# Kernel optimization log

Measured on AMD Instinct MI355X. Metric: run time of the kernel, lower is better.

The kernel has to match this reference:

```python
import jax, jax.numpy as jnp
from jax import lax
import numpy as np

B, T, D, H, L = 512, 1024, 5, 128, 16


def _u(key, shape, fan):
    bound = 1.0 / np.sqrt(fan)
    return jax.random.uniform(key, shape, jnp.float32, -bound, bound)


def setup_inputs() -> dict:
    key = jax.random.key(0)
    ks = jax.random.split(key, 16)
    return {
        "x": jax.random.normal(ks[0], (B, T, D), jnp.float32),
        # encoder GRU (PyTorch layout: rows ordered [reset; update; new])
        "enc_W_ih": _u(ks[1], (3 * H, D), H),
        "enc_W_hh": _u(ks[2], (3 * H, H), H),
        "enc_b_ih": _u(ks[3], (3 * H,), H),
        "enc_b_hh": _u(ks[4], (3 * H,), H),
        # encoder_fc: hidden -> latent
        "enc_fc_W": _u(ks[5], (L, H), H),
        "enc_fc_b": _u(ks[6], (L,), H),
        # decoder_fc: latent -> hidden
        "dec_fc_W": _u(ks[7], (H, L), L),
        "dec_fc_b": _u(ks[8], (H,), L),
        # decoder GRU (input size = hidden_dim)
        "dec_W_ih": _u(ks[9], (3 * H, H), H),
        "dec_W_hh": _u(ks[10], (3 * H, H), H),
        "dec_b_ih": _u(ks[11], (3 * H,), H),
        "dec_b_hh": _u(ks[12], (3 * H,), H),
        # output_fc: hidden -> input_dim
        "out_W": _u(ks[13], (D, H), H),
        "out_b": _u(ks[14], (D,), H),
    }


def _gru_step(W_hh, b_hh, h, xp):
    # xp: precomputed input projection [B, 3H]; PyTorch GRU cell math
    hp = h @ W_hh.T + b_hh
    r = jax.nn.sigmoid(xp[:, :H] + hp[:, :H])
    zg = jax.nn.sigmoid(xp[:, H:2 * H] + hp[:, H:2 * H])
    n = jnp.tanh(xp[:, 2 * H:] + r * hp[:, 2 * H:])
    return (1.0 - zg) * n + zg * h


def reference(x, enc_W_ih, enc_W_hh, enc_b_ih, enc_b_hh, enc_fc_W, enc_fc_b,
              dec_fc_W, dec_fc_b, dec_W_ih, dec_W_hh, dec_b_ih, dec_b_hh,
              out_W, out_b):
    b, t, _ = x.shape
    # ---- encode: precompute all input projections, scan the recurrence ----
    xp_enc = jnp.einsum('btd,gd->tbg', x, enc_W_ih) + enc_b_ih  # [T,B,3H]
    h0 = jnp.zeros((b, H), x.dtype)
    h_n, _ = lax.scan(lambda h, xp: (_gru_step(enc_W_hh, enc_b_hh, h, xp), None),
                      h0, xp_enc)
    z = h_n @ enc_fc_W.T + enc_fc_b  # [B,L]
    # ---- decode: constant repeated input => one shared input projection ----
    h_dec_in = z @ dec_fc_W.T + dec_fc_b  # [B,H]
    xp_dec = h_dec_in @ dec_W_ih.T + dec_b_ih  # [B,3H], same every step

    def dec_step(h, _):
        h_new = _gru_step(dec_W_hh, dec_b_hh, h, xp_dec)
        return h_new, h_new

    _, hs = lax.scan(dec_step, jnp.zeros((b, H), x.dtype), None, length=t)  # [T,B,H]
    recon = jnp.einsum('tbh,dh->btd', hs, out_W) + out_b  # [B,T,D]
    return recon, z
```

## Files before the change

### kernel.cpp

```cpp
#include <hip/hip_runtime.h>

#define Hd 128
#define HF 64
#define Tn 1024
#define Dn 5
#define Ln 16
#define Bn 512

__device__ __forceinline__ float sigm(float x) { return 1.0f / (1.0f + __expf(-x)); }
__device__ __forceinline__ float tanh_fast(float x) { return 1.0f - 2.0f / (1.0f + __expf(2.0f * x)); }

__global__ __launch_bounds__(512, 2) void gru_ae_kernel(
    const float* __restrict__ x,
    const float* __restrict__ eWih, const float* __restrict__ eWhh,
    const float* __restrict__ ebih, const float* __restrict__ ebhh,
    const float* __restrict__ efcW, const float* __restrict__ efcb,
    const float* __restrict__ dfcW, const float* __restrict__ dfcb,
    const float* __restrict__ dWih, const float* __restrict__ dWhh,
    const float* __restrict__ dbih, const float* __restrict__ dbhh,
    const float* __restrict__ oW, const float* __restrict__ ob,
    float* __restrict__ out)
{
    __shared__ __align__(16) float henc[2][2][Hd];
    __shared__ __align__(16) float hs[2][32][Hd];
    __shared__ __align__(16) float hdi[2][Hd];
    __shared__ float zl[2][Ln];

    const int tid  = threadIdx.x;
    const int bl   = tid >> 8;
    const int loc  = tid & 255;
    const int j    = loc >> 1;
    const int kk   = loc & 1;
    const int b    = blockIdx.x * 2 + bl;
    const int koff = kk * HF;

    float4 wr[16], wz[16], wn[16];
    {
        const float4* p0 = (const float4*)(eWhh + (size_t)j * Hd + koff);
        const float4* p1 = (const float4*)(eWhh + (size_t)(Hd + j) * Hd + koff);
        const float4* p2 = (const float4*)(eWhh + (size_t)(2 * Hd + j) * Hd + koff);
#pragma unroll
        for (int k = 0; k < 16; ++k) { wr[k] = p0[k]; wz[k] = p1[k]; wn[k] = p2[k]; }
    }
    float wir[5], wiz[5], win[5];
#pragma unroll
    for (int d = 0; d < 5; ++d) {
        wir[d] = eWih[(size_t)j * Dn + d];
        wiz[d] = eWih[(size_t)(Hd + j) * Dn + d];
        win[d] = eWih[(size_t)(2 * Hd + j) * Dn + d];
    }
    float bR = ebih[j] + ebhh[j];
    float bZ = ebih[Hd + j] + ebhh[Hd + j];
    float bihn = ebih[2 * Hd + j];
    float bhhn = ebhh[2 * Hd + j];

    if (loc < Hd) { henc[0][bl][loc] = 0.f; henc[1][bl][loc] = 0.f; }
    __syncthreads();

    float h_self = 0.f;
    int p = 0;
    const float* xrow = x + (size_t)b * Tn * Dn;
    float xc0 = xrow[0], xc1 = xrow[1], xc2 = xrow[2], xc3 = xrow[3], xc4 = xrow[4];

#pragma unroll 1
    for (int t = 0; t < Tn; ++t) {
        const int tn = (t + 1 < Tn) ? (t + 1) : t;
        const float* xq = xrow + tn * Dn;
        float nx0 = xq[0], nx1 = xq[1], nx2 = xq[2], nx3 = xq[3], nx4 = xq[4];

        float xpr = wir[0]*xc0 + wir[1]*xc1 + wir[2]*xc2 + wir[3]*xc3 + wir[4]*xc4;
        float xpz = wiz[0]*xc0 + wiz[1]*xc1 + wiz[2]*xc2 + wiz[3]*xc3 + wiz[4]*xc4;
        float xpn = win[0]*xc0 + win[1]*xc1 + win[2]*xc2 + win[3]*xc3 + win[4]*xc4;

        const float4* hv = (const float4*)&henc[p][bl][koff];
        float ar = 0.f, az = 0.f, an = 0.f;
#pragma unroll
        for (int k = 0; k < 16; ++k) {
            float4 h4 = hv[k];
            ar = fmaf(wr[k].x, h4.x, ar); az = fmaf(wz[k].x, h4.x, az); an = fmaf(wn[k].x, h4.x, an);
            ar = fmaf(wr[k].y, h4.y, ar); az = fmaf(wz[k].y, h4.y, az); an = fmaf(wn[k].y, h4.y, an);
            ar = fmaf(wr[k].z, h4.z, ar); az = fmaf(wz[k].z, h4.z, az); an = fmaf(wn[k].z, h4.z, an);
            ar = fmaf(wr[k].w, h4.w, ar); az = fmaf(wz[k].w, h4.w, az); an = fmaf(wn[k].w, h4.w, an);
        }
        ar += __shfl_xor(ar, 1); az += __shfl_xor(az, 1); an += __shfl_xor(an, 1);
        float r  = sigm(xpr + ar + bR);
        float zg = sigm(xpz + az + bZ);
        float n  = tanh_fast(xpn + bihn + r * (an + bhhn));
        float hnew = fmaf(zg, h_self - n, n);
        h_self = hnew;
        if (!kk) henc[p ^ 1][bl][j] = hnew;
        xc0 = nx0; xc1 = nx1; xc2 = nx2; xc3 = nx3; xc4 = nx4;
        __syncthreads();
        p ^= 1;
    }

    if (loc < Ln) {
        const float4* wp = (const float4*)(efcW + (size_t)loc * Hd);
        const float4* hv = (const float4*)henc[p][bl];
        float acc = efcb[loc];
#pragma unroll
        for (int k = 0; k < 32; ++k) {
            float4 w4 = wp[k], h4 = hv[k];
            acc = fmaf(w4.x, h4.x, fmaf(w4.y, h4.y, fmaf(w4.z, h4.z, fmaf(w4.w, h4.w, acc))));
        }
        out[(size_t)Bn * Tn * Dn + (size_t)b * Ln + loc] = acc;
        zl[bl][loc] = acc;
    }
    __syncthreads();

    if (loc < Hd) {
        const float4* wp = (const float4*)(dfcW + (size_t)loc * Ln);
        float acc = dfcb[loc];
#pragma unroll
        for (int l = 0; l < 4; ++l) {
            float4 w4 = wp[l];
            acc = fmaf(w4.x, zl[bl][4*l+0], acc);
            acc = fmaf(w4.y, zl[bl][4*l+1], acc);
            acc = fmaf(w4.z, zl[bl][4*l+2], acc);
            acc = fmaf(w4.w, zl[bl][4*l+3], acc);
        }
        hdi[bl][loc] = acc;
    }
    __syncthreads();

    float xdr, xdz, xdn;
    {
        const float4* p0 = (const float4*)(dWih + (size_t)j * Hd + koff);
        const float4* p1 = (const float4*)(dWih + (size_t)(Hd + j) * Hd + koff);
        const float4* p2 = (const float4*)(dWih + (size_t)(2 * Hd + j) * Hd + koff);
#pragma unroll
        for (int k = 0; k < 16; ++k) { wr[k] = p0[k]; wz[k] = p1[k]; wn[k] = p2[k]; }
        const float4* hv = (const float4*)&hdi[bl][koff];
        float a0 = 0.f, a1 = 0.f, a2 = 0.f;
#pragma unroll
        for (int k = 0; k < 16; ++k) {
            float4 h4 = hv[k];
            a0 = fmaf(wr[k].x, h4.x, a0); a1 = fmaf(wz[k].x, h4.x, a1); a2 = fmaf(wn[k].x, h4.x, a2);
            a0 = fmaf(wr[k].y, h4.y, a0); a1 = fmaf(wz[k].y, h4.y, a1); a2 = fmaf(wn[k].y, h4.y, a2);
            a0 = fmaf(wr[k].z, h4.z, a0); a1 = fmaf(wz[k].z, h4.z, a1); a2 = fmaf(wn[k].z, h4.z, a2);
            a0 = fmaf(wr[k].w, h4.w, a0); a1 = fmaf(wz[k].w, h4.w, a1); a2 = fmaf(wn[k].w, h4.w, a2);
        }
        a0 += __shfl_xor(a0, 1); a1 += __shfl_xor(a1, 1); a2 += __shfl_xor(a2, 1);
        xdr = a0 + dbih[j];
        xdz = a1 + dbih[Hd + j];
        xdn = a2 + dbih[2 * Hd + j];
    }

    {
        const float4* p0 = (const float4*)(dWhh + (size_t)j * Hd + koff);
        const float4* p1 = (const float4*)(dWhh + (size_t)(Hd + j) * Hd + koff);
        const float4* p2 = (const float4*)(dWhh + (size_t)(2 * Hd + j) * Hd + koff);
#pragma unroll
        for (int k = 0; k < 16; ++k) { wr[k] = p0[k]; wz[k] = p1[k]; wn[k] = p2[k]; }
    }
    bR = dbhh[j];
    bZ = dbhh[Hd + j];
    bhhn = dbhh[2 * Hd + j];

    if (loc < Hd) hs[bl][31][loc] = 0.f;
    h_self = 0.f;
    __syncthreads();

#pragma unroll 1
    for (int s0 = 0; s0 < Tn; s0 += 32) {
#pragma unroll 1
        for (int ss = 0; ss < 32; ++ss) {
            const int ip = (ss + 31) & 31;
            const float4* hv = (const float4*)&hs[bl][ip][koff];
            float ar = 0.f, az = 0.f, an = 0.f;
#pragma unroll
            for (int k = 0; k < 16; ++k) {
                float4 h4 = hv[k];
                ar = fmaf(wr[k].x, h4.x, ar); az = fmaf(wz[k].x, h4.x, az); an = fmaf(wn[k].x, h4.x, an);
                ar = fmaf(wr[k].y, h4.y, ar); az = fmaf(wz[k].y, h4.y, az); an = fmaf(wn[k].y, h4.y, an);
                ar = fmaf(wr[k].z, h4.z, ar); az = fmaf(wz[k].z, h4.z, az); an = fmaf(wn[k].z, h4.z, an);
                ar = fmaf(wr[k].w, h4.w, ar); az = fmaf(wz[k].w, h4.w, az); an = fmaf(wn[k].w, h4.w, an);
            }
            ar += __shfl_xor(ar, 1); az += __shfl_xor(az, 1); an += __shfl_xor(an, 1);
            float r  = sigm(xdr + ar + bR);
            float zg = sigm(xdz + az + bZ);
            float n  = tanh_fast(xdn + r * (an + bhhn));
            float hnew = fmaf(zg, h_self - n, n);
            h_self = hnew;
            if (!kk) hs[bl][ss][j] = hnew;
            __syncthreads();
        }

        if (tid < 320) {
            const int rowp = tid / 160, o = tid % 160;
            const int i = o / 5, d = o % 5;
            const float4* wrow = (const float4*)(oW + (size_t)d * Hd);
            const float4* hrow = (const float4*)hs[rowp][i];
            float ac0 = ob[d], ac1 = 0.f;
#pragma unroll
            for (int q = 0; q < 32; q += 2) {
                const int qa = (q + i) & 31, qb = (q + 1 + i) & 31;
                float4 ha = hrow[qa], wa = wrow[qa];
                float4 hb = hrow[qb], wb = wrow[qb];
                ac0 = fmaf(wa.x, ha.x, fmaf(wa.y, ha.y, fmaf(wa.z, ha.z, fmaf(wa.w, ha.w, ac0))));
                ac1 = fmaf(wb.x, hb.x, fmaf(wb.y, hb.y, fmaf(wb.z, hb.z, fmaf(wb.w, hb.w, ac1))));
            }
            out[((size_t)(blockIdx.x * 2 + rowp) * Tn + s0 + i) * Dn + d] = ac0 + ac1;
        }
        __syncthreads();
    }
}

extern "C" void kernel_launch(void* const* d_in, const int* in_sizes, int n_in,
                              void* d_out, int out_size, void* d_ws, size_t ws_size,
                              hipStream_t stream) {
    const float* x    = (const float*)d_in[0];
    const float* eWih = (const float*)d_in[1];
    const float* eWhh = (const float*)d_in[2];
    const float* ebih = (const float*)d_in[3];
    const float* ebhh = (const float*)d_in[4];
    const float* efcW = (const float*)d_in[5];
    const float* efcb = (const float*)d_in[6];
    const float* dfcW = (const float*)d_in[7];
    const float* dfcb = (const float*)d_in[8];
    const float* dWih = (const float*)d_in[9];
    const float* dWhh = (const float*)d_in[10];
    const float* dbih = (const float*)d_in[11];
    const float* dbhh = (const float*)d_in[12];
    const float* oW   = (const float*)d_in[13];
    const float* ob   = (const float*)d_in[14];
    float* out = (float*)d_out;

    gru_ae_kernel<<<dim3(Bn / 2), dim3(512), 0, stream>>>(
        x, eWih, eWhh, ebih, ebhh, efcW, efcb, dfcW, dfcb,
        dWih, dWhh, dbih, dbhh, oW, ob, out);
}
```

Baseline: 2.448 ms.

## Split GRU hidden dot products four ways with one batch row per block

Each block now handles a single batch row instead of two. The 128-wide recurrent dot product is split across 4 lanes instead of 2, which halves the per-thread weight registers and doubles the grid to 512 blocks. LDS rows are padded with a GF/CF skew to avoid bank conflicts on the quarter-sliced reads, and the 5-dim input projection is spread across the lanes and reduced together with the recurrent sums. The aim is a shorter per-step serial FMA chain and more waves per EU. In exchange, each step needs an extra shuffle-reduction stage, and block-level barriers are paid for half as many rows per block.

```diff
diff --git a/kernel.cpp b/kernel.cpp
--- a/kernel.cpp
+++ b/kernel.cpp
@@ -1,16 +1,23 @@
 #include <hip/hip_runtime.h>
 
 #define Hd 128
-#define HF 64
 #define Tn 1024
 #define Dn 5
 #define Ln 16
 #define Bn 512
+#define QP 36
+#define HP4 144
+#define GF(f) ((f) + (((f) >> 5) << 2))
+#define CF(q) (QP * ((q) >> 3) + 4 * ((q) & 7))
 
 __device__ __forceinline__ float sigm(float x) { return 1.0f / (1.0f + __expf(-x)); }
 __device__ __forceinline__ float tanh_fast(float x) { return 1.0f - 2.0f / (1.0f + __expf(2.0f * x)); }
 
-__global__ __launch_bounds__(512, 2) void gru_ae_kernel(
+#define RED4(v) { v += __shfl_xor(v, 1); v += __shfl_xor(v, 2); }
+
+__global__ __launch_bounds__(512)
+__attribute__((amdgpu_waves_per_eu(4, 4)))
+void gru_ae_kernel(
     const float* __restrict__ x,
     const float* __restrict__ eWih, const float* __restrict__ eWhh,
     const float* __restrict__ ebih, const float* __restrict__ ebhh,
@@ -21,105 +28,105 @@
     const float* __restrict__ oW, const float* __restrict__ ob,
     float* __restrict__ out)
 {
-    __shared__ __align__(16) float henc[2][2][Hd];
-    __shared__ __align__(16) float hs[2][32][Hd];
-    __shared__ __align__(16) float hdi[2][Hd];
-    __shared__ float zl[2][Ln];
-
-    const int tid  = threadIdx.x;
-    const int bl   = tid >> 8;
-    const int loc  = tid & 255;
-    const int j    = loc >> 1;
-    const int kk   = loc & 1;
-    const int b    = blockIdx.x * 2 + bl;
-    const int koff = kk * HF;
-
-    float4 wr[16], wz[16], wn[16];
+    __shared__ __align__(16) float henc[2][HP4];
+    __shared__ __align__(16) float hs[32][HP4];
+    __shared__ __align__(16) float hdi[HP4];
+    __shared__ float zl[Ln];
+
+    const int tid = threadIdx.x;
+    const int j   = tid >> 2;
+    const int kq  = tid & 3;
+    const int b   = blockIdx.x;
+    const int koff = kq * 32;
+    const int klds = kq * QP;
+
+    float4 wr[8], wz[8], wn[8];
     {
         const float4* p0 = (const float4*)(eWhh + (size_t)j * Hd + koff);
         const float4* p1 = (const float4*)(eWhh + (size_t)(Hd + j) * Hd + koff);
         const float4* p2 = (const float4*)(eWhh + (size_t)(2 * Hd + j) * Hd + koff);
 #pragma unroll
-        for (int k = 0; k < 16; ++k) { wr[k] = p0[k]; wz[k] = p1[k]; wn[k] = p2[k]; }
-    }
-    float wir[5], wiz[5], win[5];
-#pragma unroll
-    for (int d = 0; d < 5; ++d) {
-        wir[d] = eWih[(size_t)j * Dn + d];
-        wiz[d] = eWih[(size_t)(Hd + j) * Dn + d];
-        win[d] = eWih[(size_t)(2 * Hd + j) * Dn + d];
-    }
+        for (int k = 0; k < 8; ++k) { wr[k] = p0[k]; wz[k] = p1[k]; wn[k] = p2[k]; }
+    }
+    const int d0s = (kq == 1) ? 2 : (kq == 2) ? 4 : 0;
+    const int inc = (kq < 2) ? 1 : 0;
+    const float m0 = (kq < 3) ? 1.f : 0.f, m1 = (kq < 2) ? 1.f : 0.f;
+    float wxr0 = m0 * eWih[(size_t)j * Dn + d0s];
+    float wxr1 = m1 * eWih[(size_t)j * Dn + d0s + inc];
+    float wxz0 = m0 * eWih[(size_t)(Hd + j) * Dn + d0s];
+    float wxz1 = m1 * eWih[(size_t)(Hd + j) * Dn + d0s + inc];
+    float wxn0 = m0 * eWih[(size_t)(2 * Hd + j) * Dn + d0s];
+    float wxn1 = m1 * eWih[(size_t)(2 * Hd + j) * Dn + d0s + inc];
+
     float bR = ebih[j] + ebhh[j];
     float bZ = ebih[Hd + j] + ebhh[Hd + j];
     float bihn = ebih[2 * Hd + j];
     float bhhn = ebhh[2 * Hd + j];
 
-    if (loc < Hd) { henc[0][bl][loc] = 0.f; henc[1][bl][loc] = 0.f; }
+    if (tid < Hd) { henc[0][GF(tid)] = 0.f; henc[1][GF(tid)] = 0.f; }
     __syncthreads();
 
     float h_self = 0.f;
     int p = 0;
     const float* xrow = x + (size_t)b * Tn * Dn;
-    float xc0 = xrow[0], xc1 = xrow[1], xc2 = xrow[2], xc3 = xrow[3], xc4 = xrow[4];
+    float xc0 = xrow[d0s], xc1 = xrow[d0s + inc];
 
 #pragma unroll 1
     for (int t = 0; t < Tn; ++t) {
-        const int tn = (t + 1 < Tn) ? (t + 1) : t;
-        const float* xq = xrow + tn * Dn;
-        float nx0 = xq[0], nx1 = xq[1], nx2 = xq[2], nx3 = xq[3], nx4 = xq[4];
-
-        float xpr = wir[0]*xc0 + wir[1]*xc1 + wir[2]*xc2 + wir[3]*xc3 + wir[4]*xc4;
-        float xpz = wiz[0]*xc0 + wiz[1]*xc1 + wiz[2]*xc2 + wiz[3]*xc3 + wiz[4]*xc4;
-        float xpn = win[0]*xc0 + win[1]*xc1 + win[2]*xc2 + win[3]*xc3 + win[4]*xc4;
-
-        const float4* hv = (const float4*)&henc[p][bl][koff];
-        float ar = 0.f, az = 0.f, an = 0.f;
-#pragma unroll
-        for (int k = 0; k < 16; ++k) {
+        const int off = ((t + 1 < Tn) ? (t + 1) : (Tn - 1)) * Dn;
+        float nx0 = xrow[off + d0s], nx1 = xrow[off + d0s + inc];
+
+        const float4* hv = (const float4*)&henc[p][klds];
+        float ar = 0.f, az = 0.f, nh = 0.f;
+#pragma unroll
+        for (int k = 0; k < 8; ++k) {
             float4 h4 = hv[k];
-            ar = fmaf(wr[k].x, h4.x, ar); az = fmaf(wz[k].x, h4.x, az); an = fmaf(wn[k].x, h4.x, an);
-            ar = fmaf(wr[k].y, h4.y, ar); az = fmaf(wz[k].y, h4.y, az); an = fmaf(wn[k].y, h4.y, an);
-            ar = fmaf(wr[k].z, h4.z, ar); az = fmaf(wz[k].z, h4.z, az); an = fmaf(wn[k].z, h4.z, an);
-            ar = fmaf(wr[k].w, h4.w, ar); az = fmaf(wz[k].w, h4.w, az); an = fmaf(wn[k].w, h4.w, an);
-        }
-        ar += __shfl_xor(ar, 1); az += __shfl_xor(az, 1); an += __shfl_xor(an, 1);
-        float r  = sigm(xpr + ar + bR);
-        float zg = sigm(xpz + az + bZ);
-        float n  = tanh_fast(xpn + bihn + r * (an + bhhn));
+            ar = fmaf(wr[k].x, h4.x, ar); az = fmaf(wz[k].x, h4.x, az); nh = fmaf(wn[k].x, h4.x, nh);
+            ar = fmaf(wr[k].y, h4.y, ar); az = fmaf(wz[k].y, h4.y, az); nh = fmaf(wn[k].y, h4.y, nh);
+            ar = fmaf(wr[k].z, h4.z, ar); az = fmaf(wz[k].z, h4.z, az); nh = fmaf(wn[k].z, h4.z, nh);
+            ar = fmaf(wr[k].w, h4.w, ar); az = fmaf(wz[k].w, h4.w, az); nh = fmaf(wn[k].w, h4.w, nh);
+        }
+        ar = fmaf(wxr0, xc0, fmaf(wxr1, xc1, ar));
+        az = fmaf(wxz0, xc0, fmaf(wxz1, xc1, az));
+        float nx = fmaf(wxn0, xc0, wxn1 * xc1);
+        RED4(ar); RED4(az); RED4(nh); RED4(nx);
+        float r  = sigm(ar + bR);
+        float zg = sigm(az + bZ);
+        float n  = tanh_fast(nx + bihn + r * (nh + bhhn));
         float hnew = fmaf(zg, h_self - n, n);
         h_self = hnew;
-        if (!kk) henc[p ^ 1][bl][j] = hnew;
-        xc0 = nx0; xc1 = nx1; xc2 = nx2; xc3 = nx3; xc4 = nx4;
+        if (!kq) henc[p ^ 1][GF(j)] = hnew;
+        xc0 = nx0; xc1 = nx1;
         __syncthreads();
         p ^= 1;
     }
 
-    if (loc < Ln) {
-        const float4* wp = (const float4*)(efcW + (size_t)loc * Hd);
-        const float4* hv = (const float4*)henc[p][bl];
-        float acc = efcb[loc];
-#pragma unroll
-        for (int k = 0; k < 32; ++k) {
-            float4 w4 = wp[k], h4 = hv[k];
+    if (tid < Ln) {
+        const float4* wp = (const float4*)(efcW + (size_t)tid * Hd);
+        float acc = efcb[tid];
+#pragma unroll
+        for (int q = 0; q < 32; ++q) {
+            float4 w4 = wp[q];
+            float4 h4 = *(const float4*)&henc[p][CF(q)];
             acc = fmaf(w4.x, h4.x, fmaf(w4.y, h4.y, fmaf(w4.z, h4.z, fmaf(w4.w, h4.w, acc))));
         }
-        out[(size_t)Bn * Tn * Dn + (size_t)b * Ln + loc] = acc;
-        zl[bl][loc] = acc;
-    }
-    __syncthreads();
-
-    if (loc < Hd) {
-        const float4* wp = (const float4*)(dfcW + (size_t)loc * Ln);
-        float acc = dfcb[loc];
+        out[(size_t)Bn * Tn * Dn + (size_t)b * Ln + tid] = acc;
+        zl[tid] = acc;
+    }
+    __syncthreads();
+
+    if (tid < Hd) {
+        const float4* wp = (const float4*)(dfcW + (size_t)tid * Ln);
+        float acc = dfcb[tid];
 #pragma unroll
         for (int l = 0; l < 4; ++l) {
             float4 w4 = wp[l];
-            acc = fmaf(w4.x, zl[bl][4*l+0], acc);
-            acc = fmaf(w4.y, zl[bl][4*l+1], acc);
-            acc = fmaf(w4.z, zl[bl][4*l+2], acc);
-            acc = fmaf(w4.w, zl[bl][4*l+3], acc);
-        }
-        hdi[bl][loc] = acc;
+            acc = fmaf(w4.x, zl[4 * l + 0], acc);
+            acc = fmaf(w4.y, zl[4 * l + 1], acc);
+            acc = fmaf(w4.z, zl[4 * l + 2], acc);
+            acc = fmaf(w4.w, zl[4 * l + 3], acc);
+        }
+        hdi[GF(tid)] = acc;
     }
     __syncthreads();
 
@@ -129,21 +136,22 @@
         const float4* p1 = (const float4*)(dWih + (size_t)(Hd + j) * Hd + koff);
         const float4* p2 = (const float4*)(dWih + (size_t)(2 * Hd + j) * Hd + koff);
 #pragma unroll
-        for (int k = 0; k < 16; ++k) { wr[k] = p0[k]; wz[k] = p1[k]; wn[k] = p2[k]; }
-        const float4* hv = (const float4*)&hdi[bl][koff];
+        for (int k = 0; k < 8; ++k) { wr[k] = p0[k]; wz[k] = p1[k]; wn[k] = p2[k]; }
+        const float4* hv = (const float4*)&hdi[klds];
         float a0 = 0.f, a1 = 0.f, a2 = 0.f;
 #pragma unroll
-        for (int k = 0; k < 16; ++k) {
+        for (int k = 0; k < 8; ++k) {
             float4 h4 = hv[k];
             a0 = fmaf(wr[k].x, h4.x, a0); a1 = fmaf(wz[k].x, h4.x, a1); a2 = fmaf(wn[k].x, h4.x, a2);
             a0 = fmaf(wr[k].y, h4.y, a0); a1 = fmaf(wz[k].y, h4.y, a1); a2 = fmaf(wn[k].y, h4.y, a2);
             a0 = fmaf(wr[k].z, h4.z, a0); a1 = fmaf(wz[k].z, h4.z, a1); a2 = fmaf(wn[k].z, h4.z, a2);
             a0 = fmaf(wr[k].w, h4.w, a0); a1 = fmaf(wz[k].w, h4.w, a1); a2 = fmaf(wn[k].w, h4.w, a2);
         }
-        a0 += __shfl_xor(a0, 1); a1 += __shfl_xor(a1, 1); a2 += __shfl_xor(a2, 1);
-        xdr = a0 + dbih[j];
-        xdz = a1 + dbih[Hd + j];
+        RED4(a0); RED4(a1); RED4(a2);
+        xdr = a0 + dbih[j] + dbhh[j];
+        xdz = a1 + dbih[Hd + j] + dbhh[Hd + j];
         xdn = a2 + dbih[2 * Hd + j];
+        bhhn = dbhh[2 * Hd + j];
     }
 
     {
@@ -151,13 +159,10 @@
         const float4* p1 = (const float4*)(dWhh + (size_t)(Hd + j) * Hd + koff);
         const float4* p2 = (const float4*)(dWhh + (size_t)(2 * Hd + j) * Hd + koff);
 #pragma unroll
-        for (int k = 0; k < 16; ++k) { wr[k] = p0[k]; wz[k] = p1[k]; wn[k] = p2[k]; }
-    }
-    bR = dbhh[j];
-    bZ = dbhh[Hd + j];
-    bhhn = dbhh[2 * Hd + j];
-
-    if (loc < Hd) hs[bl][31][loc] = 0.f;
+        for (int k = 0; k < 8; ++k) { wr[k] = p0[k]; wz[k] = p1[k]; wn[k] = p2[k]; }
+    }
+
+    if (tid < Hd) hs[31][GF(tid)] = 0.f;
     h_self = 0.f;
     __syncthreads();
 
@@ -166,41 +171,41 @@
 #pragma unroll 1
         for (int ss = 0; ss < 32; ++ss) {
             const int ip = (ss + 31) & 31;
-            const float4* hv = (const float4*)&hs[bl][ip][koff];
-            float ar = 0.f, az = 0.f, an = 0.f;
-#pragma unroll
-            for (int k = 0; k < 16; ++k) {
+            const float4* hv = (const float4*)&hs[ip][klds];
+            float ar = 0.f, az = 0.f, nh = 0.f;
+#pragma unroll
+            for (int k = 0; k < 8; ++k) {
                 float4 h4 = hv[k];
-                ar = fmaf(wr[k].x, h4.x, ar); az = fmaf(wz[k].x, h4.x, az); an = fmaf(wn[k].x, h4.x, an);
-                ar = fmaf(wr[k].y, h4.y, ar); az = fmaf(wz[k].y, h4.y, az); an = fmaf(wn[k].y, h4.y, an);
-                ar = fmaf(wr[k].z, h4.z, ar); az = fmaf(wz[k].z, h4.z, az); an = fmaf(wn[k].z, h4.z, an);
-                ar = fmaf(wr[k].w, h4.w, ar); az = fmaf(wz[k].w, h4.w, az); an = fmaf(wn[k].w, h4.w, an);
+                ar = fmaf(wr[k].x, h4.x, ar); az = fmaf(wz[k].x, h4.x, az); nh = fmaf(wn[k].x, h4.x, nh);
+                ar = fmaf(wr[k].y, h4.y, ar); az = fmaf(wz[k].y, h4.y, az); nh = fmaf(wn[k].y, h4.y, nh);
+                ar = fmaf(wr[k].z, h4.z, ar); az = fmaf(wz[k].z, h4.z, az); nh = fmaf(wn[k].z, h4.z, nh);
+                ar = fmaf(wr[k].w, h4.w, ar); az = fmaf(wz[k].w, h4.w, az); nh = fmaf(wn[k].w, h4.w, nh);
             }
-            ar += __shfl_xor(ar, 1); az += __shfl_xor(az, 1); an += __shfl_xor(an, 1);
-            float r  = sigm(xdr + ar + bR);
-            float zg = sigm(xdz + az + bZ);
-            float n  = tanh_fast(xdn + r * (an + bhhn));
+            RED4(ar); RED4(az); RED4(nh);
+            float r  = sigm(xdr + ar);
+            float zg = sigm(xdz + az);
+            float n  = tanh_fast(xdn + r * (nh + bhhn));
             float hnew = fmaf(zg, h_self - n, n);
             h_self = hnew;
-            if (!kk) hs[bl][ss][j] = hnew;
+            if (!kq) hs[ss][GF(j)] = hnew;
             __syncthreads();
         }
 
-        if (tid < 320) {
-            const int rowp = tid / 160, o = tid % 160;
-            const int i = o / 5, d = o % 5;
+        if (tid < 160) {
+            const int i = tid / 5, d = tid % 5;
             const float4* wrow = (const float4*)(oW + (size_t)d * Hd);
-            const float4* hrow = (const float4*)hs[rowp][i];
             float ac0 = ob[d], ac1 = 0.f;
 #pragma unroll
             for (int q = 0; q < 32; q += 2) {
                 const int qa = (q + i) & 31, qb = (q + 1 + i) & 31;
-                float4 ha = hrow[qa], wa = wrow[qa];
-                float4 hb = hrow[qb], wb = wrow[qb];
+                float4 ha = *(const float4*)&hs[i][CF(qa)];
+                float4 wa = wrow[qa];
+                float4 hb = *(const float4*)&hs[i][CF(qb)];
+                float4 wb = wrow[qb];
                 ac0 = fmaf(wa.x, ha.x, fmaf(wa.y, ha.y, fmaf(wa.z, ha.z, fmaf(wa.w, ha.w, ac0))));
                 ac1 = fmaf(wb.x, hb.x, fmaf(wb.y, hb.y, fmaf(wb.z, hb.z, fmaf(wb.w, hb.w, ac1))));
             }
-            out[((size_t)(blockIdx.x * 2 + rowp) * Tn + s0 + i) * Dn + d] = ac0 + ac1;
+            out[((size_t)b * Tn + s0 + i) * Dn + d] = ac0 + ac1;
         }
         __syncthreads();
     }
@@ -226,7 +231,7 @@
     const float* ob   = (const float*)d_in[14];
     float* out = (float*)d_out;
 
-    gru_ae_kernel<<<dim3(Bn / 2), dim3(512), 0, stream>>>(
+    gru_ae_kernel<<<dim3(Bn), dim3(512), 0, stream>>>(
         x, eWih, eWhh, ebih, ebhh, efcW, efcb, dfcW, dfcb,
         dWih, dWhh, dbih, dbhh, oW, ob, out);
 }
```

Measured after the change: 2.551 ms. 4.2% more time.
